# Kernel optimization log

Measured on AMD Instinct MI355X. Metric: run time of the kernel, lower is better.

The kernel has to match this reference:

```python
import jax, jax.numpy as jnp
import numpy as np

NUM_BATCH, NUM_OBJ, NUM_DBOX, NUM_CLASSES = 64, 50, 8732, 2
JACCARD_THRESH = 0.5
NEGPOS_RATIO = 3
VARIANCE = (0.1, 0.2)


def setup_inputs() -> dict:
    key = jax.random.key(0)
    k1, k2, k3, k4, k5, k6 = jax.random.split(key, 6)
    loc_data = jax.random.normal(k1, (NUM_BATCH, NUM_DBOX, 4), dtype=jnp.float32)
    conf_data = jax.random.normal(k2, (NUM_BATCH, NUM_DBOX, NUM_CLASSES), dtype=jnp.float32)
    # default boxes in center-size form (cx, cy, w, h)
    cxcy = jax.random.uniform(k3, (NUM_DBOX, 2), minval=0.05, maxval=0.95)
    wh = jax.random.uniform(k4, (NUM_DBOX, 2), minval=0.05, maxval=0.4)
    dbox_list = jnp.concatenate([cxcy, wh], axis=1).astype(jnp.float32)
    # ground-truth boxes in point form [xmin,ymin,xmax,ymax] plus label (class 0 -> conf label 1)
    tc = jax.random.uniform(k5, (NUM_BATCH, NUM_OBJ, 2), minval=0.15, maxval=0.85)
    twh = jax.random.uniform(k6, (NUM_BATCH, NUM_OBJ, 2), minval=0.05, maxval=0.3)
    truths = jnp.concatenate([tc - twh / 2, tc + twh / 2], axis=-1)
    labels = jnp.zeros((NUM_BATCH, NUM_OBJ, 1), dtype=jnp.float32)
    targets = jnp.concatenate([truths, labels], axis=-1).astype(jnp.float32)
    return {"loc_data": loc_data, "conf_data": conf_data, "dbox_list": dbox_list, "targets": targets}


def point_form(boxes):
    # (cx,cy,w,h) -> (xmin,ymin,xmax,ymax)
    return jnp.concatenate([boxes[:, :2] - boxes[:, 2:] / 2, boxes[:, :2] + boxes[:, 2:] / 2], axis=1)


def jaccard(a, b):
    # a: [No,4], b: [Nd,4], both point form -> [No,Nd]
    lt = jnp.maximum(a[:, None, :2], b[None, :, :2])
    rb = jnp.minimum(a[:, None, 2:], b[None, :, 2:])
    wh = jnp.clip(rb - lt, 0.0)
    inter = wh[..., 0] * wh[..., 1]
    area_a = ((a[:, 2] - a[:, 0]) * (a[:, 3] - a[:, 1]))[:, None]
    area_b = ((b[:, 2] - b[:, 0]) * (b[:, 3] - b[:, 1]))[None, :]
    return inter / (area_a + area_b - inter)


def encode(matched, priors):
    # matched: [Nd,4] point form; priors: [Nd,4] center-size form
    g_cxcy = (matched[:, :2] + matched[:, 2:]) / 2 - priors[:, :2]
    g_cxcy = g_cxcy / (VARIANCE[0] * priors[:, 2:])
    g_wh = jnp.log((matched[:, 2:] - matched[:, :2]) / priors[:, 2:]) / VARIANCE[1]
    return jnp.concatenate([g_cxcy, g_wh], axis=1)


def match_one(truths, labels, dbox):
    # truths [No,4], labels [No], dbox [Nd,4] center-size
    overlaps = jaccard(truths, point_form(dbox))  # [No, Nd]
    best_prior_idx = jnp.argmax(overlaps, axis=1)          # [No]
    best_truth_overlap = jnp.max(overlaps, axis=0)          # [Nd]
    best_truth_idx = jnp.argmax(overlaps, axis=0)           # [Nd]
    best_truth_overlap = best_truth_overlap.at[best_prior_idx].set(2.0)
    best_truth_idx = best_truth_idx.at[best_prior_idx].set(jnp.arange(truths.shape[0]))
    matched = truths[best_truth_idx]                        # [Nd,4]
    conf = labels[best_truth_idx].astype(jnp.int32) + 1
    conf = jnp.where(best_truth_overlap < JACCARD_THRESH, 0, conf)
    loc = encode(matched, dbox)
    return loc, conf


def smooth_l1(x, t):
    d = jnp.abs(x - t)
    return jnp.where(d < 1.0, 0.5 * d * d, d - 0.5)


def cross_entropy(logits, labels):
    # logits [..., C], labels [...] int -> elementwise CE
    logp = jax.nn.log_softmax(logits, axis=-1)
    return -jnp.take_along_axis(logp, labels[..., None], axis=-1)[..., 0]


def reference(loc_data, conf_data, dbox_list, targets):
    num_batch, num_dbox, _ = loc_data.shape
    truths = targets[..., :-1]        # [B,No,4]
    labels = targets[..., -1]          # [B,No]
    loc_t, conf_t_label = jax.vmap(match_one, in_axes=(0, 0, None))(truths, labels, dbox_list)
    pos_mask = conf_t_label > 0        # [B,Nd]

    # localization loss: smooth L1 over positive priors, mean over selected elements
    l1 = smooth_l1(loc_data, loc_t)                               # [B,Nd,4]
    n_pos_elems = 4.0 * jnp.sum(pos_mask)
    loss_l = jnp.nan_to_num(jnp.sum(l1 * pos_mask[..., None]) / n_pos_elems)

    # per-prior confidence loss for hard-negative mining
    ce = cross_entropy(conf_data, conf_t_label)                   # [B,Nd]
    ce_mined = jnp.where(pos_mask, 0.0, ce)
    loss_idx = jnp.argsort(-ce_mined, axis=1)                     # descending sort
    idx_rank = jnp.argsort(loss_idx, axis=1)
    num_pos = jnp.sum(pos_mask, axis=1, keepdims=True)            # [B,1]
    num_neg = jnp.clip(num_pos * NEGPOS_RATIO, 20, num_dbox)
    neg_mask = idx_rank < num_neg                                 # [B,Nd]

    posf = pos_mask.astype(ce.dtype)
    negf = neg_mask.astype(ce.dtype)
    loss_c_pos = jnp.nan_to_num(jnp.sum(ce * posf) / jnp.sum(posf))
    loss_c_neg = jnp.nan_to_num(jnp.sum(ce * negf) / jnp.sum(negf))
    loss_c = loss_c_pos + loss_c_neg
    return jnp.stack([loss_l, loss_c, loss_c_pos, loss_c_neg])
```

## Files before the change

kernel.cpp:

```cpp
#include <hip/hip_runtime.h>

#define NB     64
#define NOBJ   50
#define ND     8732
#define PPT    2
#define BLK1   256
#define PRB    (BLK1*PPT)
#define NSPLIT 18
#define NW1    (BLK1/64)
#define NPART  NSPLIT
#define CHUNK  10
#define NCHUNK 5
#define BLK2   1024
#define NW2    (BLK2/64)
#define ITER2  ((ND+BLK2-1)/BLK2)
#define ND4    (ND/4)

__device__ float              g_part[NB*5];
__device__ float4             g_ce4[(size_t)NB*ND4];
__device__ unsigned long long g_keys[(size_t)NB*NPART*NOBJ];
__device__ int                g_hist[(size_t)NB*NSPLIT*256];
__device__ float              g_bp[NB*NSPLIT*3];
__device__ int                g_done;

__device__ __forceinline__ float iou_rn(float px1,float py1,float px2,float py2,float pa,
                                        float tx1,float ty1,float tx2,float ty2,float ta){
    float ltx=fmaxf(tx1,px1), lty=fmaxf(ty1,py1);
    float rbx=fminf(tx2,px2), rby=fminf(ty2,py2);
    float ww=fmaxf(__fsub_rn(rbx,ltx),0.f), hh=fmaxf(__fsub_rn(rby,lty),0.f);
    float inter=__fmul_rn(ww,hh);
    return __fdividef(inter, __fsub_rn(__fadd_rn(ta,pa),inter));
}
__device__ __forceinline__ float lse2(float x0,float x1){
    float m=fmaxf(x0,x1);
    return m+__logf(__expf(x0-m)+__expf(x1-m));
}
__device__ __forceinline__ float sl1_enc(float4 p,float tx1,float ty1,float tx2,float ty2,float4 ld){
    float g0=((tx1+tx2)*0.5f-p.x)/(0.1f*p.z);
    float g1=((ty1+ty2)*0.5f-p.y)/(0.1f*p.w);
    float g2=__logf((tx2-tx1)/p.z)*5.0f;
    float g3=__logf((ty2-ty1)/p.w)*5.0f;
    float t0=fabsf(ld.x-g0),t1=fabsf(ld.y-g1),t2=fabsf(ld.z-g2),t3=fabsf(ld.w-g3);
    return (t0<1.f?0.5f*t0*t0:t0-0.5f)+(t1<1.f?0.5f*t1*t1:t1-0.5f)
          +(t2<1.f?0.5f*t2*t2:t2-0.5f)+(t3<1.f?0.5f*t3*t3:t3-0.5f);
}

__global__ __launch_bounds__(BLK1) void k1(const float* __restrict__ loc_data,
                                           const float* __restrict__ conf_data,
                                           const float* __restrict__ dbox,
                                           const float* __restrict__ targets){
    __shared__ float s_tx1[NOBJ],s_ty1[NOBJ],s_tx2[NOBJ],s_ty2[NOBJ],s_lab[NOBJ];
    __shared__ unsigned long long s_wk[NW1][NOBJ];
    __shared__ int   s_wh[NW1*256];
    __shared__ float s_r1[NW1],s_r2[NW1],s_r3[NW1];
    const int blk=blockIdx.x, b=blk/NSPLIT, spl=blk%NSPLIT;
    const int tid=threadIdx.x, lane=tid&63, wv=tid>>6;
    if (blk==0 && tid==0) g_done=0;
    if (tid<NOBJ){
        const float* t=targets+(b*NOBJ+tid)*5;
        s_tx1[tid]=t[0];s_ty1[tid]=t[1];s_tx2[tid]=t[2];s_ty2[tid]=t[3];s_lab[tid]=t[4];
    }
    for (int i=tid;i<NW1*256;i+=BLK1) s_wh[i]=0;

    const int d0=spl*PRB;
    const int cnt=(ND-d0<PRB)?(ND-d0):PRB;
    float px1[PPT],py1[PPT],px2[PPT],py2[PPT],pa[PPT];
    bool vld[PPT]; float bov[PPT]; int bj[PPT];
#pragma unroll
    for (int q=0;q<PPT;++q){
        int dl=tid*PPT+q; vld[q]=dl<cnt; bov[q]=-1.f; bj[q]=0;
        px1[q]=py1[q]=px2[q]=py2[q]=pa[q]=0.f;
        if (vld[q]){
            float4 p=reinterpret_cast<const float4*>(dbox)[d0+dl];
            float hw=__fmul_rn(0.5f,p.z), hh=__fmul_rn(0.5f,p.w);
            px1[q]=__fsub_rn(p.x,hw); py1[q]=__fsub_rn(p.y,hh);
            px2[q]=__fadd_rn(p.x,hw); py2[q]=__fadd_rn(p.y,hh);
            pa[q]=__fmul_rn(p.z,p.w);
        }
    }

    const float* tg = targets + (size_t)b*NOBJ*5;
    for (int c=0;c<NCHUNK;++c){
        float tx1c[CHUNK],ty1c[CHUNK],tx2c[CHUNK],ty2c[CHUNK],tac[CHUNK];
#pragma unroll
        for (int jj=0;jj<CHUNK;++jj){
            int j=c*CHUNK+jj;
            tx1c[jj]=tg[j*5+0]; ty1c[jj]=tg[j*5+1];
            tx2c[jj]=tg[j*5+2]; ty2c[jj]=tg[j*5+3];
            tac[jj]=__fmul_rn(__fsub_rn(tx2c[jj],tx1c[jj]),__fsub_rn(ty2c[jj],ty1c[jj]));
        }
        float tb[CHUNK]; int td[CHUNK];
#pragma unroll
        for (int jj=0;jj<CHUNK;++jj){tb[jj]=-1.f;td[jj]=0;}
#pragma unroll
        for (int q=0;q<PPT;++q){
            if (!vld[q]) continue;
            const int d=d0+tid*PPT+q;
#pragma unroll
            for (int jj=0;jj<CHUNK;++jj){
                float iou=iou_rn(px1[q],py1[q],px2[q],py2[q],pa[q],
                                 tx1c[jj],ty1c[jj],tx2c[jj],ty2c[jj],tac[jj]);
                if (iou>bov[q]){bov[q]=iou;bj[q]=c*CHUNK+jj;}
                if (iou>tb[jj]){tb[jj]=iou;td[jj]=d;}
            }
        }
#pragma unroll
        for (int jj=0;jj<CHUNK;++jj){
            float m=tb[jj];
#pragma unroll
            for (int off=32;off>=1;off>>=1) m=fmaxf(m,__shfl_xor(m,off,64));
            unsigned long long msk=__ballot(tb[jj]==m);
            int lead=__builtin_ctzll(msk);
            int dwin=__shfl(td[jj],lead,64);
            if (lane==0){
                s_wk[wv][c*CHUNK+jj]=(m>=0.f)
                    ?(((unsigned long long)__float_as_uint(m)<<32)
                      |(unsigned long long)(0xFFFFFFFFu-(unsigned)dwin))
                    :0ull;
            }
        }
    }
    __syncthreads();
    if (tid<NOBJ){
        unsigned long long m=s_wk[0][tid];
        for (int w=1;w<NW1;++w){unsigned long long o=s_wk[w][tid]; if(o>m)m=o;}
        g_keys[((size_t)b*NSPLIT+spl)*NOBJ+tid]=m;
    }

    float np=0.f,sl=0.f,sc=0.f;
    float raw[PPT]={0.f,0.f};
    if (vld[0]){
        float4 cf4=reinterpret_cast<const float4*>(conf_data)[((size_t)b*ND+d0)/2+tid];
#pragma unroll
        for (int q=0;q<PPT;++q){
            const int d=d0+tid*PPT+q;
            float cfx=(q==0)?cf4.x:cf4.z, cfy=(q==0)?cf4.y:cf4.w;
            float l=lse2(cfx,cfy);
            bool pos=!(bov[q]<0.5f);
            int jb=bj[q];
            int lab=pos?((int)s_lab[jb]+1):0;
            float cev=l-(lab>=1?cfy:cfx);
            raw[q]=pos?-cev:cev;
            atomicAdd(&s_wh[wv*256+(int)(__float_as_uint(fmaxf(raw[q],0.f))>>24)],1);
            if (pos){
                np+=1.f; sc+=cev;
                float4 p=reinterpret_cast<const float4*>(dbox)[d];
                float4 ldv=reinterpret_cast<const float4*>(loc_data)[(size_t)b*ND+d];
                sl+=sl1_enc(p,s_tx1[jb],s_ty1[jb],s_tx2[jb],s_ty2[jb],ldv);
            }
        }
        float2 st; st.x=raw[0]; st.y=raw[1];
        reinterpret_cast<float2*>(g_ce4)[((size_t)b*ND+d0)/2+tid]=st;
    }
#pragma unroll
    for (int off=32;off>=1;off>>=1){
        np+=__shfl_xor(np,off,64); sl+=__shfl_xor(sl,off,64); sc+=__shfl_xor(sc,off,64);
    }
    if (lane==0){s_r1[wv]=np;s_r2[wv]=sl;s_r3[wv]=sc;}
    __syncthreads();
    if (tid==0){
        float a=0.f,bb2=0.f,cc=0.f;
        for (int w=0;w<NW1;++w){a+=s_r1[w];bb2+=s_r2[w];cc+=s_r3[w];}
        g_bp[(b*NSPLIT+spl)*3+0]=a;
        g_bp[(b*NSPLIT+spl)*3+1]=bb2;
        g_bp[(b*NSPLIT+spl)*3+2]=cc;
    }
    {
        int s=0;
        for (int w=0;w<NW1;++w) s+=s_wh[w*256+tid];
        g_hist[(size_t)(b*NSPLIT+spl)*256+tid]=s;
    }
}

__global__ __launch_bounds__(BLK2) void k2(const float* __restrict__ loc_data,
                                           const float* __restrict__ conf_data,
                                           const float* __restrict__ dbox,
                                           const float* __restrict__ targets,
                                           float* __restrict__ out){
    __shared__ float4 s_ce4[ND4];
    __shared__ unsigned long long s_km[NOBJ*16];
    __shared__ unsigned int s_dj[NOBJ];
    __shared__ float s_tx1[NOBJ],s_ty1[NOBJ],s_tx2[NOBJ],s_ty2[NOBJ],s_ta[NOBJ],s_lab[NOBJ];
    __shared__ int   s_hist[256];
    __shared__ int   s_wh[NW2*256];
    __shared__ float s_bpl[NSPLIT*3];
    __shared__ float s_rf[NW2]; __shared__ int s_ri[NW2];
    __shared__ int   s_wt[4];
    __shared__ float s_dnp,s_dsl,s_dsc;
    __shared__ int   s_sel,s_krem,s_kk,s_last;
    float* s_ce=(float*)s_ce4;

    const int b=blockIdx.x, tid=threadIdx.x, lane=tid&63, wv=tid>>6;

    if (tid<NOBJ){
        const float* t=targets+(b*NOBJ+tid)*5;
        float x1=t[0],y1=t[1],x2=t[2],y2=t[3];
        s_tx1[tid]=x1;s_ty1[tid]=y1;s_tx2[tid]=x2;s_ty2[tid]=y2;
        s_ta[tid]=__fmul_rn(__fsub_rn(x2,x1),__fsub_rn(y2,y1));
        s_lab[tid]=t[4];
    }
    if (tid<NOBJ*16){
        int j=tid>>4, s=tid&15;
        const unsigned long long* kp=g_keys+(size_t)b*NPART*NOBJ;
        unsigned long long m=kp[(size_t)s*NOBJ+j];
        if (s+16<NPART){unsigned long long o=kp[(size_t)(s+16)*NOBJ+j]; if(o>m)m=o;}
        s_km[tid]=m;
    }
    for (int i=tid;i<ND4;i+=BLK2) s_ce4[i]=g_ce4[(size_t)b*ND4+i];
    if (tid<256){
        int s=0;
        for (int sp=0;sp<NSPLIT;++sp) s+=g_hist[(size_t)(b*NSPLIT+sp)*256+tid];
        s_hist[tid]=s;
    }
    if (tid<NSPLIT*3) s_bpl[tid]=g_bp[b*NSPLIT*3+tid];
    __syncthreads();
    if (tid<NOBJ){
        unsigned long long m=s_km[tid*16];
        for (int s=1;s<16;++s){unsigned long long o=s_km[tid*16+s]; if(o>m)m=o;}
        s_dj[tid]=0xFFFFFFFFu-(unsigned)(m&0xFFFFFFFFull);
    }
    __syncthreads();

    float dnp=0.f,dsl=0.f,dsc=0.f;
    if (tid<NOBJ){
        unsigned d=s_dj[tid]; bool win=true;
        for (int j2=tid+1;j2<NOBJ;++j2) if (s_dj[j2]==d){win=false;break;}
        if (win){
            float4 p=reinterpret_cast<const float4*>(dbox)[d];
            float hw=__fmul_rn(0.5f,p.z), hh2=__fmul_rn(0.5f,p.w);
            float ppx1=__fsub_rn(p.x,hw),ppy1=__fsub_rn(p.y,hh2);
            float ppx2=__fadd_rn(p.x,hw),ppy2=__fadd_rn(p.y,hh2);
            float ppa=__fmul_rn(p.z,p.w);
            float bov=-1.f; int jb=0;
            for (int j=0;j<NOBJ;++j){
                float iou=iou_rn(ppx1,ppy1,ppx2,ppy2,ppa,
                                 s_tx1[j],s_ty1[j],s_tx2[j],s_ty2[j],s_ta[j]);
                if (iou>bov){bov=iou;jb=j;}
            }
            bool oldpos=!(bov<0.5f);
            float2 cf=reinterpret_cast<const float2*>(conf_data)[(size_t)b*ND+d];
            float l=lse2(cf.x,cf.y);
            float4 ldv=reinterpret_cast<const float4*>(loc_data)[(size_t)b*ND+d];
            int labN=(int)s_lab[tid]+1;
            float ceN=l-(labN>=1?cf.y:cf.x);
            dsc+=ceN; dsl+=sl1_enc(p,s_tx1[tid],s_ty1[tid],s_tx2[tid],s_ty2[tid],ldv);
            if (oldpos){
                int labO=(int)s_lab[jb]+1;
                float ceO=l-(labO>=1?cf.y:cf.x);
                dsc-=ceO; dsl-=sl1_enc(p,s_tx1[jb],s_ty1[jb],s_tx2[jb],s_ty2[jb],ldv);
            } else dnp+=1.f;
            float oldraw=s_ce[d];
            atomicAdd(&s_hist[(int)(__float_as_uint(fmaxf(oldraw,0.f))>>24)],-1);
            atomicAdd(&s_hist[0],1);
            s_ce[d]=-ceN;
        }
    }
    if (wv==0){
#pragma unroll
        for (int off=32;off>=1;off>>=1){
            dnp+=__shfl_xor(dnp,off,64); dsl+=__shfl_xor(dsl,off,64); dsc+=__shfl_xor(dsc,off,64);
        }
        if (lane==0){s_dnp=dnp;s_dsl=dsl;s_dsc=dsc;}
    }
    __syncthreads();
    if (tid==0){
        float np=s_dnp, sl=s_dsl, sc=s_dsc;
        for (int i=0;i<NSPLIT;++i){np+=s_bpl[i*3];sl+=s_bpl[i*3+1];sc+=s_bpl[i*3+2];}
        int npi=(int)np; int k=npi*3; if(k<20)k=20; if(k>ND)k=ND;
        s_kk=k;
        g_part[b*5+0]=np; g_part[b*5+1]=sl; g_part[b*5+2]=sc; g_part[b*5+3]=(float)k;
    }
    __syncthreads();
    const int k=s_kk;

    unsigned prefix=0u,pmask=0u; int krem=k;
    for (int p=0;p<3;++p){
        const int shift=24-p*8;
        int cnt=0;
        if (p==0){
            if (tid<256) cnt=s_hist[tid];
        } else {
            for (int i=tid;i<NW2*256;i+=BLK2) s_wh[i]=0;
            __syncthreads();
            for (int it=0;it<ITER2;++it){
                int d=tid+it*BLK2;
                if (d<ND){
                    unsigned vb=__float_as_uint(fmaxf(s_ce[d],0.f));
                    if ((vb&pmask)==prefix)
                        atomicAdd(&s_wh[wv*256+(int)((vb>>shift)&255u)],1);
                }
            }
            __syncthreads();
            if (tid<256){
                for (int w=0;w<NW2;++w) cnt+=s_wh[w*256+tid];
            }
        }
        int S=cnt,add=0;
        if (tid<256){
#pragma unroll
            for (int off=1;off<64;off<<=1){
                int t=__shfl_down(S,off,64);
                if (lane+off<64) S+=t;
            }
            if (lane==0) s_wt[wv]=S;
        }
        __syncthreads();
        if (tid<256){
            for (int w=wv+1;w<4;++w) add+=s_wt[w];
            S+=add;
            int Snext=__shfl_down(S,1,64);
            if (lane==63) Snext=add;
            if (S>=krem && Snext<krem){s_sel=tid;s_krem=krem-(S-cnt);}
        }
        __syncthreads();
        prefix|=((unsigned)s_sel)<<shift;
        pmask|=255u<<shift;
        krem=s_krem;
        __syncthreads();
    }
    const float T=__uint_as_float(prefix);

    int cgt=0; float sgt=0.f;
    for (int it=0;it<ITER2;++it){
        int d=tid+it*BLK2;
        if (d<ND){
            float v=fmaxf(s_ce[d],0.f);
            if (v>T){cgt++;sgt+=v;}
        }
    }
#pragma unroll
    for (int off=32;off>=1;off>>=1){cgt+=__shfl_xor(cgt,off,64);sgt+=__shfl_xor(sgt,off,64);}
    if (lane==0){s_ri[wv]=cgt;s_rf[wv]=sgt;}
    __syncthreads();
    if (tid==0){
        int cg=0; float sg=0.f;
        for (int w=0;w<NW2;++w){cg+=s_ri[w];sg+=s_rf[w];}
        int need=k-cg;
        float stk=sg+(float)need*T;
        if (!(T>0.f)&&need>0){
            int taken=0;
            for (int d=0;d<ND&&taken<need;++d){
                float r=s_ce[d];
                if (!(r>0.f)){stk+=fabsf(r);++taken;}
            }
        }
        g_part[b*5+4]=stk;
    }

    if (tid==0){__threadfence(); int old=atomicAdd(&g_done,1); s_last=(old==NB-1)?1:0;}
    __syncthreads();
    if (s_last&&tid<NB){
        __threadfence();
        volatile float* gp=g_part;
        float np=gp[tid*5+0],sl=gp[tid*5+1],sc=gp[tid*5+2],kk=gp[tid*5+3],st=gp[tid*5+4];
#pragma unroll
        for (int off=32;off>=1;off>>=1){
            np+=__shfl_xor(np,off,64);sl+=__shfl_xor(sl,off,64);
            sc+=__shfl_xor(sc,off,64);kk+=__shfl_xor(kk,off,64);st+=__shfl_xor(st,off,64);
        }
        if (tid==0){
            float loss_l=(np>0.f)?sl/(4.f*np):0.f;
            float lcp=(np>0.f)?sc/np:0.f;
            float lcn=(kk>0.f)?st/kk:0.f;
            out[0]=loss_l;out[1]=lcp+lcn;out[2]=lcp;out[3]=lcn;
        }
    }
}

extern "C" void kernel_launch(void* const* d_in, const int* in_sizes, int n_in,
                              void* d_out, int out_size, void* d_ws, size_t ws_size,
                              hipStream_t stream) {
    const float* loc     = (const float*)d_in[0];
    const float* conf    = (const float*)d_in[1];
    const float* dboxp   = (const float*)d_in[2];
    const float* targets = (const float*)d_in[3];
    float* out = (float*)d_out;

    k1<<<NB*NSPLIT, BLK1, 0, stream>>>(loc, conf, dboxp, targets);
    k2<<<NB, BLK2, 0, stream>>>(loc, conf, dboxp, targets, out);
}
```

Baseline: 136.9 us.

## Split k1 into prior-matching and per-truth best-prior blocks

k1 now runs two kinds of blocks in one grid. Prior-side blocks handle 4 priors per thread and compute only each prior's best truth plus the CE and loss partials. Separate truth-side blocks have each wavefront scan all priors, staged in shared-memory tiles, to find the best prior for one truth, so the per-chunk wave reductions disappear. This also removes the cross-split key merge in k2, at the cost of each truth-side block recomputing prior boxes and doing a serial scan over 8732 priors.

```diff
diff --git a/kernel.cpp b/kernel.cpp
--- a/kernel.cpp
+++ b/kernel.cpp
@@ -3,14 +3,15 @@
 #define NB     64
 #define NOBJ   50
 #define ND     8732
-#define PPT    2
-#define BLK1   256
-#define PRB    (BLK1*PPT)
-#define NSPLIT 18
-#define NW1    (BLK1/64)
-#define NPART  NSPLIT
-#define CHUNK  10
-#define NCHUNK 5
+#define BLK    256
+#define NW     (BLK/64)
+#define PPT    4
+#define PRB    (BLK*PPT)
+#define NBA    9
+#define TB     13
+#define GRID   (NB*NBA + NB*TB)
+#define TILE   1024
+#define NTILE  ((ND + TILE - 1)/TILE)
 #define BLK2   1024
 #define NW2    (BLK2/64)
 #define ITER2  ((ND+BLK2-1)/BLK2)
@@ -18,9 +19,9 @@
 
 __device__ float              g_part[NB*5];
 __device__ float4             g_ce4[(size_t)NB*ND4];
-__device__ unsigned long long g_keys[(size_t)NB*NPART*NOBJ];
-__device__ int                g_hist[(size_t)NB*NSPLIT*256];
-__device__ float              g_bp[NB*NSPLIT*3];
+__device__ unsigned long long g_keys[NB*NOBJ];
+__device__ int                g_hist[(size_t)NB*NBA*256];
+__device__ float              g_bp[NB*NBA*3];
 __device__ int                g_done;
 
 __device__ __forceinline__ float iou_rn(float px1,float py1,float px2,float py2,float pa,
@@ -45,130 +46,156 @@
           +(t2<1.f?0.5f*t2*t2:t2-0.5f)+(t3<1.f?0.5f*t3*t3:t3-0.5f);
 }
 
-__global__ __launch_bounds__(BLK1) void k1(const float* __restrict__ loc_data,
-                                           const float* __restrict__ conf_data,
-                                           const float* __restrict__ dbox,
-                                           const float* __restrict__ targets){
+__global__ __launch_bounds__(BLK) void k1(const float* __restrict__ loc_data,
+                                          const float* __restrict__ conf_data,
+                                          const float* __restrict__ dbox,
+                                          const float* __restrict__ targets){
     __shared__ float s_tx1[NOBJ],s_ty1[NOBJ],s_tx2[NOBJ],s_ty2[NOBJ],s_lab[NOBJ];
-    __shared__ unsigned long long s_wk[NW1][NOBJ];
-    __shared__ int   s_wh[NW1*256];
-    __shared__ float s_r1[NW1],s_r2[NW1],s_r3[NW1];
-    const int blk=blockIdx.x, b=blk/NSPLIT, spl=blk%NSPLIT;
-    const int tid=threadIdx.x, lane=tid&63, wv=tid>>6;
+    __shared__ int   s_wh[NW*256];
+    __shared__ float s_r1[NW],s_r2[NW],s_r3[NW];
+    __shared__ float s_px1[TILE],s_py1[TILE],s_px2[TILE],s_py2[TILE],s_pa[TILE];
+
+    const int blk=blockIdx.x, tid=threadIdx.x, lane=tid&63, wv=tid>>6;
+    const float4* dbox4=reinterpret_cast<const float4*>(dbox);
     if (blk==0 && tid==0) g_done=0;
-    if (tid<NOBJ){
-        const float* t=targets+(b*NOBJ+tid)*5;
-        s_tx1[tid]=t[0];s_ty1[tid]=t[1];s_tx2[tid]=t[2];s_ty2[tid]=t[3];s_lab[tid]=t[4];
-    }
-    for (int i=tid;i<NW1*256;i+=BLK1) s_wh[i]=0;
-
-    const int d0=spl*PRB;
-    const int cnt=(ND-d0<PRB)?(ND-d0):PRB;
-    float px1[PPT],py1[PPT],px2[PPT],py2[PPT],pa[PPT];
-    bool vld[PPT]; float bov[PPT]; int bj[PPT];
-#pragma unroll
-    for (int q=0;q<PPT;++q){
-        int dl=tid*PPT+q; vld[q]=dl<cnt; bov[q]=-1.f; bj[q]=0;
-        px1[q]=py1[q]=px2[q]=py2[q]=pa[q]=0.f;
-        if (vld[q]){
-            float4 p=reinterpret_cast<const float4*>(dbox)[d0+dl];
-            float hw=__fmul_rn(0.5f,p.z), hh=__fmul_rn(0.5f,p.w);
-            px1[q]=__fsub_rn(p.x,hw); py1[q]=__fsub_rn(p.y,hh);
-            px2[q]=__fadd_rn(p.x,hw); py2[q]=__fadd_rn(p.y,hh);
-            pa[q]=__fmul_rn(p.z,p.w);
-        }
-    }
-
-    const float* tg = targets + (size_t)b*NOBJ*5;
-    for (int c=0;c<NCHUNK;++c){
-        float tx1c[CHUNK],ty1c[CHUNK],tx2c[CHUNK],ty2c[CHUNK],tac[CHUNK];
-#pragma unroll
-        for (int jj=0;jj<CHUNK;++jj){
-            int j=c*CHUNK+jj;
-            tx1c[jj]=tg[j*5+0]; ty1c[jj]=tg[j*5+1];
-            tx2c[jj]=tg[j*5+2]; ty2c[jj]=tg[j*5+3];
-            tac[jj]=__fmul_rn(__fsub_rn(tx2c[jj],tx1c[jj]),__fsub_rn(ty2c[jj],ty1c[jj]));
-        }
-        float tb[CHUNK]; int td[CHUNK];
-#pragma unroll
-        for (int jj=0;jj<CHUNK;++jj){tb[jj]=-1.f;td[jj]=0;}
+
+    if (blk < NB*NBA) {
+        const int b=blk/NBA, spl=blk%NBA;
+        if (tid<NOBJ){
+            const float* t=targets+(b*NOBJ+tid)*5;
+            s_tx1[tid]=t[0];s_ty1[tid]=t[1];s_tx2[tid]=t[2];s_ty2[tid]=t[3];s_lab[tid]=t[4];
+        }
+        for (int i=tid;i<NW*256;i+=BLK) s_wh[i]=0;
+        __syncthreads();
+
+        const int d0=spl*PRB;
+        const bool vld=(d0+tid*PPT)<ND;
+        float px1[PPT],py1[PPT],px2[PPT],py2[PPT],pa[PPT];
+        float bov[PPT]; int bj[PPT];
 #pragma unroll
         for (int q=0;q<PPT;++q){
-            if (!vld[q]) continue;
-            const int d=d0+tid*PPT+q;
-#pragma unroll
-            for (int jj=0;jj<CHUNK;++jj){
-                float iou=iou_rn(px1[q],py1[q],px2[q],py2[q],pa[q],
-                                 tx1c[jj],ty1c[jj],tx2c[jj],ty2c[jj],tac[jj]);
-                if (iou>bov[q]){bov[q]=iou;bj[q]=c*CHUNK+jj;}
-                if (iou>tb[jj]){tb[jj]=iou;td[jj]=d;}
-            }
-        }
-#pragma unroll
-        for (int jj=0;jj<CHUNK;++jj){
-            float m=tb[jj];
-#pragma unroll
-            for (int off=32;off>=1;off>>=1) m=fmaxf(m,__shfl_xor(m,off,64));
-            unsigned long long msk=__ballot(tb[jj]==m);
-            int lead=__builtin_ctzll(msk);
-            int dwin=__shfl(td[jj],lead,64);
-            if (lane==0){
-                s_wk[wv][c*CHUNK+jj]=(m>=0.f)
-                    ?(((unsigned long long)__float_as_uint(m)<<32)
-                      |(unsigned long long)(0xFFFFFFFFu-(unsigned)dwin))
-                    :0ull;
-            }
-        }
-    }
-    __syncthreads();
-    if (tid<NOBJ){
-        unsigned long long m=s_wk[0][tid];
-        for (int w=1;w<NW1;++w){unsigned long long o=s_wk[w][tid]; if(o>m)m=o;}
-        g_keys[((size_t)b*NSPLIT+spl)*NOBJ+tid]=m;
-    }
-
-    float np=0.f,sl=0.f,sc=0.f;
-    float raw[PPT]={0.f,0.f};
-    if (vld[0]){
-        float4 cf4=reinterpret_cast<const float4*>(conf_data)[((size_t)b*ND+d0)/2+tid];
-#pragma unroll
-        for (int q=0;q<PPT;++q){
-            const int d=d0+tid*PPT+q;
-            float cfx=(q==0)?cf4.x:cf4.z, cfy=(q==0)?cf4.y:cf4.w;
-            float l=lse2(cfx,cfy);
-            bool pos=!(bov[q]<0.5f);
-            int jb=bj[q];
-            int lab=pos?((int)s_lab[jb]+1):0;
-            float cev=l-(lab>=1?cfy:cfx);
-            raw[q]=pos?-cev:cev;
-            atomicAdd(&s_wh[wv*256+(int)(__float_as_uint(fmaxf(raw[q],0.f))>>24)],1);
-            if (pos){
-                np+=1.f; sc+=cev;
-                float4 p=reinterpret_cast<const float4*>(dbox)[d];
-                float4 ldv=reinterpret_cast<const float4*>(loc_data)[(size_t)b*ND+d];
-                sl+=sl1_enc(p,s_tx1[jb],s_ty1[jb],s_tx2[jb],s_ty2[jb],ldv);
-            }
-        }
-        float2 st; st.x=raw[0]; st.y=raw[1];
-        reinterpret_cast<float2*>(g_ce4)[((size_t)b*ND+d0)/2+tid]=st;
-    }
-#pragma unroll
-    for (int off=32;off>=1;off>>=1){
-        np+=__shfl_xor(np,off,64); sl+=__shfl_xor(sl,off,64); sc+=__shfl_xor(sc,off,64);
-    }
-    if (lane==0){s_r1[wv]=np;s_r2[wv]=sl;s_r3[wv]=sc;}
-    __syncthreads();
-    if (tid==0){
-        float a=0.f,bb2=0.f,cc=0.f;
-        for (int w=0;w<NW1;++w){a+=s_r1[w];bb2+=s_r2[w];cc+=s_r3[w];}
-        g_bp[(b*NSPLIT+spl)*3+0]=a;
-        g_bp[(b*NSPLIT+spl)*3+1]=bb2;
-        g_bp[(b*NSPLIT+spl)*3+2]=cc;
-    }
-    {
-        int s=0;
-        for (int w=0;w<NW1;++w) s+=s_wh[w*256+tid];
-        g_hist[(size_t)(b*NSPLIT+spl)*256+tid]=s;
+            bov[q]=-1.f; bj[q]=0;
+            px1[q]=py1[q]=px2[q]=py2[q]=pa[q]=0.f;
+            if (vld){
+                float4 p=dbox4[d0+tid*PPT+q];
+                float hw=__fmul_rn(0.5f,p.z), hh=__fmul_rn(0.5f,p.w);
+                px1[q]=__fsub_rn(p.x,hw); py1[q]=__fsub_rn(p.y,hh);
+                px2[q]=__fadd_rn(p.x,hw); py2[q]=__fadd_rn(p.y,hh);
+                pa[q]=__fmul_rn(p.z,p.w);
+            }
+        }
+        const float* tg=targets+(size_t)b*NOBJ*5;
+        for (int c=0;c<5;++c){
+            float tx1c[10],ty1c[10],tx2c[10],ty2c[10],tac[10];
+#pragma unroll
+            for (int jj=0;jj<10;++jj){
+                int j=c*10+jj;
+                tx1c[jj]=tg[j*5+0]; ty1c[jj]=tg[j*5+1];
+                tx2c[jj]=tg[j*5+2]; ty2c[jj]=tg[j*5+3];
+                tac[jj]=__fmul_rn(__fsub_rn(tx2c[jj],tx1c[jj]),__fsub_rn(ty2c[jj],ty1c[jj]));
+            }
+#pragma unroll
+            for (int q=0;q<PPT;++q){
+#pragma unroll
+                for (int jj=0;jj<10;++jj){
+                    float iou=iou_rn(px1[q],py1[q],px2[q],py2[q],pa[q],
+                                     tx1c[jj],ty1c[jj],tx2c[jj],ty2c[jj],tac[jj]);
+                    if (iou>bov[q]){bov[q]=iou;bj[q]=c*10+jj;}
+                }
+            }
+        }
+        float np=0.f,sl=0.f,sc=0.f;
+        if (vld){
+            const size_t cbase=((size_t)b*ND+d0)/2;
+            float4 cfa=reinterpret_cast<const float4*>(conf_data)[cbase+tid*2];
+            float4 cfb=reinterpret_cast<const float4*>(conf_data)[cbase+tid*2+1];
+            float raw[PPT];
+#pragma unroll
+            for (int q=0;q<PPT;++q){
+                const int d=d0+tid*PPT+q;
+                float cfx=(q==0)?cfa.x:(q==1)?cfa.z:(q==2)?cfb.x:cfb.z;
+                float cfy=(q==0)?cfa.y:(q==1)?cfa.w:(q==2)?cfb.y:cfb.w;
+                float l=lse2(cfx,cfy);
+                bool pos=!(bov[q]<0.5f);
+                int jb=bj[q];
+                int lab=pos?((int)s_lab[jb]+1):0;
+                float cev=l-(lab>=1?cfy:cfx);
+                raw[q]=pos?-cev:cev;
+                atomicAdd(&s_wh[wv*256+(int)(__float_as_uint(fmaxf(raw[q],0.f))>>24)],1);
+                if (pos){
+                    np+=1.f; sc+=cev;
+                    float4 p=dbox4[d];
+                    float4 ldv=reinterpret_cast<const float4*>(loc_data)[(size_t)b*ND+d];
+                    sl+=sl1_enc(p,s_tx1[jb],s_ty1[jb],s_tx2[jb],s_ty2[jb],ldv);
+                }
+            }
+            float4 st; st.x=raw[0];st.y=raw[1];st.z=raw[2];st.w=raw[3];
+            g_ce4[((size_t)b*ND+d0)/4+tid]=st;
+        }
+#pragma unroll
+        for (int off=32;off>=1;off>>=1){
+            np+=__shfl_xor(np,off,64); sl+=__shfl_xor(sl,off,64); sc+=__shfl_xor(sc,off,64);
+        }
+        if (lane==0){s_r1[wv]=np;s_r2[wv]=sl;s_r3[wv]=sc;}
+        __syncthreads();
+        if (tid==0){
+            float a=0.f,bb=0.f,cc=0.f;
+            for (int w=0;w<NW;++w){a+=s_r1[w];bb+=s_r2[w];cc+=s_r3[w];}
+            g_bp[(b*NBA+spl)*3+0]=a;
+            g_bp[(b*NBA+spl)*3+1]=bb;
+            g_bp[(b*NBA+spl)*3+2]=cc;
+        }
+        if (tid<256){
+            int s=0;
+            for (int w=0;w<NW;++w) s+=s_wh[w*256+tid];
+            g_hist[(size_t)(b*NBA+spl)*256+tid]=s;
+        }
+    } else {
+        const int r=blk-NB*NBA;
+        const int b=r/TB;
+        const int t=(r%TB)*NW+wv;
+        const bool tv=t<NOBJ;
+        float tx1=0,ty1=0,tx2=0,ty2=0,ta=1.f;
+        if (tv){
+            const float* tt=targets+(b*NOBJ+t)*5;
+            tx1=tt[0];ty1=tt[1];tx2=tt[2];ty2=tt[3];
+            ta=__fmul_rn(__fsub_rn(tx2,tx1),__fsub_rn(ty2,ty1));
+        }
+        float bt=-1.f; int bd=0;
+        for (int tile=0;tile<NTILE;++tile){
+            const int base=tile*TILE;
+#pragma unroll
+            for (int i=0;i<TILE/BLK;++i){
+                int dl=tid+i*BLK;
+                int d=base+dl;
+                float4 p=make_float4(0.f,0.f,0.f,0.f);
+                if (d<ND) p=dbox4[d];
+                float hw=__fmul_rn(0.5f,p.z), hh=__fmul_rn(0.5f,p.w);
+                s_px1[dl]=__fsub_rn(p.x,hw); s_py1[dl]=__fsub_rn(p.y,hh);
+                s_px2[dl]=__fadd_rn(p.x,hw); s_py2[dl]=__fadd_rn(p.y,hh);
+                s_pa[dl]=__fmul_rn(p.z,p.w);
+            }
+            __syncthreads();
+            if (tv){
+#pragma unroll 4
+                for (int dd=lane;dd<TILE;dd+=64){
+                    float iou=iou_rn(s_px1[dd],s_py1[dd],s_px2[dd],s_py2[dd],s_pa[dd],
+                                     tx1,ty1,tx2,ty2,ta);
+                    if (iou>bt){bt=iou;bd=base+dd;}
+                }
+            }
+            __syncthreads();
+        }
+        if (tv){
+            unsigned long long key=((unsigned long long)__float_as_uint(bt)<<32)
+                                  |(unsigned long long)(0xFFFFFFFFu-(unsigned)bd);
+#pragma unroll
+            for (int off=32;off>=1;off>>=1){
+                unsigned long long o=__shfl_xor(key,off,64);
+                if (o>key) key=o;
+            }
+            if (lane==0) g_keys[b*NOBJ+t]=key;
+        }
     }
 }
 
@@ -178,12 +205,11 @@
                                            const float* __restrict__ targets,
                                            float* __restrict__ out){
     __shared__ float4 s_ce4[ND4];
-    __shared__ unsigned long long s_km[NOBJ*16];
     __shared__ unsigned int s_dj[NOBJ];
     __shared__ float s_tx1[NOBJ],s_ty1[NOBJ],s_tx2[NOBJ],s_ty2[NOBJ],s_ta[NOBJ],s_lab[NOBJ];
     __shared__ int   s_hist[256];
     __shared__ int   s_wh[NW2*256];
-    __shared__ float s_bpl[NSPLIT*3];
+    __shared__ float s_bpl[NBA*3];
     __shared__ float s_rf[NW2]; __shared__ int s_ri[NW2];
     __shared__ int   s_wt[4];
     __shared__ float s_dnp,s_dsl,s_dsc;
@@ -198,27 +224,15 @@
         s_tx1[tid]=x1;s_ty1[tid]=y1;s_tx2[tid]=x2;s_ty2[tid]=y2;
         s_ta[tid]=__fmul_rn(__fsub_rn(x2,x1),__fsub_rn(y2,y1));
         s_lab[tid]=t[4];
-    }
-    if (tid<NOBJ*16){
-        int j=tid>>4, s=tid&15;
-        const unsigned long long* kp=g_keys+(size_t)b*NPART*NOBJ;
-        unsigned long long m=kp[(size_t)s*NOBJ+j];
-        if (s+16<NPART){unsigned long long o=kp[(size_t)(s+16)*NOBJ+j]; if(o>m)m=o;}
-        s_km[tid]=m;
+        s_dj[tid]=0xFFFFFFFFu-(unsigned)(g_keys[b*NOBJ+tid]&0xFFFFFFFFull);
     }
     for (int i=tid;i<ND4;i+=BLK2) s_ce4[i]=g_ce4[(size_t)b*ND4+i];
     if (tid<256){
         int s=0;
-        for (int sp=0;sp<NSPLIT;++sp) s+=g_hist[(size_t)(b*NSPLIT+sp)*256+tid];
+        for (int sp=0;sp<NBA;++sp) s+=g_hist[(size_t)(b*NBA+sp)*256+tid];
         s_hist[tid]=s;
     }
-    if (tid<NSPLIT*3) s_bpl[tid]=g_bp[b*NSPLIT*3+tid];
-    __syncthreads();
-    if (tid<NOBJ){
-        unsigned long long m=s_km[tid*16];
-        for (int s=1;s<16;++s){unsigned long long o=s_km[tid*16+s]; if(o>m)m=o;}
-        s_dj[tid]=0xFFFFFFFFu-(unsigned)(m&0xFFFFFFFFull);
-    }
+    if (tid<NBA*3) s_bpl[tid]=g_bp[b*NBA*3+tid];
     __syncthreads();
 
     float dnp=0.f,dsl=0.f,dsc=0.f;
@@ -265,7 +279,7 @@
     __syncthreads();
     if (tid==0){
         float np=s_dnp, sl=s_dsl, sc=s_dsc;
-        for (int i=0;i<NSPLIT;++i){np+=s_bpl[i*3];sl+=s_bpl[i*3+1];sc+=s_bpl[i*3+2];}
+        for (int i=0;i<NBA;++i){np+=s_bpl[i*3];sl+=s_bpl[i*3+1];sc+=s_bpl[i*3+2];}
         int npi=(int)np; int k=npi*3; if(k<20)k=20; if(k>ND)k=ND;
         s_kk=k;
         g_part[b*5+0]=np; g_part[b*5+1]=sl; g_part[b*5+2]=sc; g_part[b*5+3]=(float)k;
@@ -340,8 +354,8 @@
         if (!(T>0.f)&&need>0){
             int taken=0;
             for (int d=0;d<ND&&taken<need;++d){
-                float r=s_ce[d];
-                if (!(r>0.f)){stk+=fabsf(r);++taken;}
+                float r2=s_ce[d];
+                if (!(r2>0.f)){stk+=fabsf(r2);++taken;}
             }
         }
         g_part[b*5+4]=stk;
@@ -376,6 +390,6 @@
     const float* targets = (const float*)d_in[3];
     float* out = (float*)d_out;
 
-    k1<<<NB*NSPLIT, BLK1, 0, stream>>>(loc, conf, dboxp, targets);
+    k1<<<GRID, BLK, 0, stream>>>(loc, conf, dboxp, targets);
     k2<<<NB, BLK2, 0, stream>>>(loc, conf, dboxp, targets, out);
 }
```

New measurement: 143.5 us. 4.8% more time.
